# Optimization experiments

Measured on AMD Instinct MI355X. Metric: run time of the kernel, lower is better.

Reference implementation:

```python
import jax, jax.numpy as jnp
import numpy as np

B, S, D = 4, 4096, 1024
H = 16
DH = D // H  # 64, required by the fused kernel


def setup_inputs() -> dict:
    key = jax.random.key(0)
    ks = jax.random.split(key, 5)
    scale = 1.0 / np.sqrt(D)  # xavier-ish init scale for square matrices
    return {
        "x": jax.random.normal(ks[0], (B, S, D), dtype=jnp.float32),
        "Wq": jax.random.normal(ks[1], (D, D), dtype=jnp.float32) * scale,
        "Wk": jax.random.normal(ks[2], (D, D), dtype=jnp.float32) * scale,
        "Wv": jax.random.normal(ks[3], (D, D), dtype=jnp.float32) * scale,
        "Wo": jax.random.normal(ks[4], (D, D), dtype=jnp.float32) * scale,
    }


def reference(x, Wq, Wk, Wv, Wo):
    # Fused QKV projection + linear (non-softmax) attention.
    # Q = x Wq, K = x Wk, V = x Wv, split into H heads of size DH.
    b, s, d = x.shape
    h, dh = H, d // H

    def to_heads(t):
        return t.reshape(b, s, h, dh).transpose(0, 2, 1, 3)  # [B,H,S,dh]

    q = to_heads(jnp.einsum("bsd,de->bse", x, Wq))
    k = to_heads(jnp.einsum("bsd,de->bse", x, Wk))
    v = to_heads(jnp.einsum("bsd,de->bse", x, Wv))

    # Linear attention: O(S * dh^2) per head, never materializes [S,S].
    # out = (1/sqrt(dh)) * Q @ (K^T V)
    scale = 1.0 / jnp.sqrt(jnp.asarray(dh, dtype=x.dtype))
    kv = jnp.einsum("bhsd,bhse->bhde", k, v)          # [B,H,dh,dh]
    out = jnp.einsum("bhsd,bhde->bhse", q, kv) * scale  # [B,H,S,dh]

    # kernel output [B,H,S,dh] -> transpose(1,2) -> view [B,S,D]
    out = out.transpose(0, 2, 1, 3).reshape(b, s, d)
    # out_proj: nn.Linear(D, D, bias=False) -> x @ W.T
    return jnp.einsum("bsd,ed->bse", out, Wo)
```

## Files before the change

### kernel.cpp

```cpp
#include <hip/hip_runtime.h>

typedef unsigned short u16;
typedef unsigned int u32;
typedef u16 u16x8 __attribute__((ext_vector_type(8)));
typedef u16 u16x4 __attribute__((ext_vector_type(4)));
typedef __bf16 bf16x8 __attribute__((ext_vector_type(8)));
typedef float f32x4 __attribute__((ext_vector_type(4)));

__device__ __forceinline__ u16 f2bf(float f) {
    u32 u = __builtin_bit_cast(u32, f);
    u32 r = (u + 0x7fffu + ((u >> 16) & 1u)) >> 16;
    return (u16)r;
}
__device__ __forceinline__ void async16(const u16* g, u16* lds_base) {
    __builtin_amdgcn_global_load_lds(
        (const __attribute__((address_space(1))) void*)g,
        (__attribute__((address_space(3))) void*)lds_base, 16, 0, 0);
}
template <bool SW>
__device__ __forceinline__ f32x4 mf(bf16x8 a, bf16x8 b, f32x4 c) {
    if constexpr (SW) return __builtin_amdgcn_mfma_f32_16x16x32_bf16(b, a, c, 0, 0, 0);
    else              return __builtin_amdgcn_mfma_f32_16x16x32_bf16(a, b, c, 0, 0, 0);
}

__global__ void cvt3_f32_bf16(const float* __restrict__ x, u16* __restrict__ xb,
                              const float* __restrict__ wq, u16* __restrict__ wqb,
                              const float* __restrict__ wo, u16* __restrict__ wob) {
    const int bid = blockIdx.x;
    const float* src; u16* dst; long base;
    if (bid < 8192)      { src = x;  dst = xb;  base = bid; }
    else if (bid < 8704) { src = wq; dst = wqb; base = bid - 8192; }
    else                 { src = wo; dst = wob; base = bid - 8704; }
    const long idx = (base * 256 + threadIdx.x) * 8;
    float4 a = *(const float4*)(src + idx);
    float4 b = *(const float4*)(src + idx + 4);
    u16x8 o;
    o[0] = f2bf(a.x); o[1] = f2bf(a.y); o[2] = f2bf(a.z); o[3] = f2bf(a.w);
    o[4] = f2bf(b.x); o[5] = f2bf(b.y); o[6] = f2bf(b.z); o[7] = f2bf(b.w);
    *(u16x8*)(dst + idx) = o;
}

__global__ void transpose_cvt(const float* __restrict__ W0, const float* __restrict__ W1,
                              u16* __restrict__ WT) {
    __shared__ float tile[32][33];
    const float* W = (blockIdx.z == 0) ? W0 : W1;
    int n0 = blockIdx.x * 32, k0 = blockIdx.y * 32;
    int tx = threadIdx.x, ty = threadIdx.y;
#pragma unroll
    for (int r = 0; r < 4; ++r)
        tile[ty + 8 * r][tx] = W[(size_t)(k0 + ty + 8 * r) * 1024 + n0 + tx];
    __syncthreads();
#pragma unroll
    for (int r = 0; r < 4; ++r) {
        int n = n0 + ty + 8 * r;
        WT[((size_t)blockIdx.z * 1024 + n) * 1024 + k0 + tx] = f2bf(tile[tx][ty + 8 * r]);
    }
}

#define BAR __builtin_amdgcn_s_barrier()
#define WAITLGK do { asm volatile("s_waitcnt lgkmcnt(0)" ::: "memory"); \
                     __builtin_amdgcn_sched_barrier(0); } while (0)
#define PRIO1 __builtin_amdgcn_s_setprio(1)
#define PRIO0 __builtin_amdgcn_s_setprio(0)
#define VM(n) asm volatile("s_waitcnt vmcnt(" #n ")" ::: "memory")

#define As SM[0]
#define Bs SM[1]

#define LDA(buf, mh) do { _Pragma("unroll") for (int mi = 0; mi < 4; ++mi) { \
    const int rA = (wm * 128 + (mh) * 64 + mi * 16 + frow) * 64; \
    aF[mi][0] = *(const bf16x8*)&As[buf][rA + xs0]; \
    aF[mi][1] = *(const bf16x8*)&As[buf][rA + xs1]; } } while (0)

#define LDB(buf, nh) do { _Pragma("unroll") for (int ni = 0; ni < 2; ++ni) { \
    const int rB = (wn * 64 + (nh) * 32 + ni * 16 + frow) * 64; \
    bF[(nh) * 2 + ni][0] = *(const bf16x8*)&Bs[buf][rB + xs0]; \
    bF[(nh) * 2 + ni][1] = *(const bf16x8*)&Bs[buf][rB + xs1]; } } while (0)

#define MFQ(mh, nh) do { _Pragma("unroll") for (int mi = 0; mi < 4; ++mi) \
  _Pragma("unroll") for (int ni = 0; ni < 2; ++ni) \
  _Pragma("unroll") for (int s = 0; s < 2; ++s) \
    acc[(mh) * 4 + mi][(nh) * 2 + ni] = mf<SW>( \
        aF[mi][s], bF[(nh) * 2 + ni][s], acc[(mh) * 4 + mi][(nh) * 2 + ni]); } while (0)

#define TILE4(buf, S2, S3, S4, W1, W2, WV) \
  LDA(buf, 0); LDB(buf, 0); BAR; WAITLGK; PRIO1; MFQ(0, 0); PRIO0; W1; BAR; \
  LDB(buf, 1); S2; BAR; WAITLGK; PRIO1; MFQ(0, 1); PRIO0; W2; BAR; \
  LDA(buf, 1); S3; BAR; WAITLGK; PRIO1; MFQ(1, 1); PRIO0; BAR; \
  S4; BAR; WAITLGK; PRIO1; MFQ(1, 0); PRIO0; WV; BAR;

template <typename OutT, bool KVMODE>
__global__ __launch_bounds__(512, 2) void gemm8p(
    const u16* __restrict__ A, int lda,
    const u16* __restrict__ Bt, int ldb,
    OutT* __restrict__ Cq, int ldc, int K, int nTN,
    size_t btStrideB, u16* __restrict__ Kt, u16* __restrict__ Vt) {
    constexpr bool SW = !KVMODE;
    __shared__ u16 SM[2][2][256 * 64];
    const int tid = threadIdx.x;
    const int wid = tid >> 6, lane = tid & 63;
    const int wm = wid >> 2, wn = wid & 3;

    const int nwg = gridDim.x;
    const int orig = blockIdx.x;
    const int id = (orig & 7) * (nwg >> 3) + (orig >> 3);
    const size_t mBase = (size_t)(id / nTN) * 256;
    const size_t nBase = (size_t)(id % nTN) * 256;

    if (!KVMODE) Bt += (mBase >> 12) * btStrideB;

    const int srow = lane >> 3;
    const int scol = (((lane & 7) ^ (srow & 7)) * 8);

    auto stageH = [&](int buf, int isB, int h, int kt) {
        const u16* g = isB ? Bt : A;
        const int ld = isB ? ldb : lda;
        const size_t rb = isB ? nBase : mBase;
        u16* lds = isB ? Bs[buf] : As[buf];
#pragma unroll
        for (int j = 0; j < 2; ++j) {
            const int rowL = isB ? ((wid >> 1) * 64 + h * 32 + (wid & 1) * 16 + j * 8)
                                 : ((wid >> 2) * 128 + h * 64 + (wid & 3) * 16 + j * 8);
            async16(g + (rb + rowL + srow) * (size_t)ld + (size_t)kt * 64 + scol,
                    lds + rowL * 64);
        }
    };

    const int frow = lane & 15;
    const int xs0 = (((lane >> 4)) ^ (frow & 7)) * 8;
    const int xs1 = ((4 + (lane >> 4)) ^ (frow & 7)) * 8;

    f32x4 acc[8][4] = {};
    bf16x8 aF[4][2], bF[4][2];

#pragma unroll
    for (int h = 0; h < 2; ++h) { stageH(0, 0, h, 0); stageH(0, 1, h, 0); }
#pragma unroll
    for (int h = 0; h < 2; ++h) { stageH(1, 0, h, 1); stageH(1, 1, h, 1); }
    VM(8);
    BAR;

    const int np = K >> 7;
    for (int p = 0; p < np - 1; ++p) {
        const int k2 = 2 * p + 2, k3 = 2 * p + 3;
        TILE4(0,
              { stageH(0, 0, 0, k2); stageH(0, 1, 0, k2); },
              stageH(0, 1, 1, k2),
              stageH(0, 0, 1, k2),
              VM(10), VM(12), VM(12));
        TILE4(1,
              { stageH(1, 0, 0, k3); stageH(1, 1, 0, k3); },
              stageH(1, 1, 1, k3),
              stageH(1, 0, 1, k3),
              VM(10), VM(12), VM(12));
    }
    TILE4(0, , , , , , VM(0));
    TILE4(1, , , , , , );

    const int rb4 = (lane >> 4) * 4;
    const int cx = lane & 15;
    if (!KVMODE) {
#pragma unroll
        for (int m = 0; m < 8; ++m) {
            const size_t row = mBase + wm * 128 + m * 16 + cx;
#pragma unroll
            for (int n = 0; n < 4; ++n) {
                const size_t col = nBase + wn * 64 + n * 16 + rb4;
                *(float4*)&Cq[row * (size_t)ldc + col] =
                    *(float4*)&acc[m][n];
            }
        }
    } else {
        __syncthreads();
        u16* T = &SM[0][0][0];
        const int nLoc = (int)(nBase & 1023);
#pragma unroll
        for (int n = 0; n < 4; ++n) {
            const int colL = wn * 64 + n * 16 + cx;
#pragma unroll
            for (int m = 0; m < 8; ++m) {
                const int R = wm * 128 + m * 16 + rb4;
                u16x4 v;
                v[0] = f2bf(acc[m][n][0]); v[1] = f2bf(acc[m][n][1]);
                v[2] = f2bf(acc[m][n][2]); v[3] = f2bf(acc[m][n][3]);
                const int byteoff = colL * 512 + ((((R >> 3) ^ (colL & 31)) << 4) | ((R & 7) << 1));
                *(u16x4*)((char*)T + byteoff) = v;
            }
        }
        __syncthreads();
        const int b = (int)(mBase >> 12);
        u16* KV = ((nBase >> 10) == 0 ? Kt : Vt);
        const int j = lane & 31;
#pragma unroll
        for (int u = 0; u < 16; ++u) {
            const int iLoc = wid * 32 + u * 2 + (lane >> 5);
            const int byteoff = iLoc * 512 + ((j ^ (iLoc & 31)) << 4);
            const int gcol = nLoc + iLoc;
            u16* dst = KV + (((size_t)(b * 16 + (gcol >> 6)) * 64 + (gcol & 63)) << 12)
                          + (mBase & 4095) + j * 8;
            *(u16x8*)dst = *(const u16x8*)((char*)T + byteoff);
        }
    }
}

__global__ __launch_bounds__(256, 2) void gemm128(
    const u16* __restrict__ A, int lda,
    const u16* __restrict__ Bt, int ldb,
    u16* __restrict__ C, int ldc, int K) {
    __shared__ u16 A2[2][128 * 64];
    __shared__ u16 B2[2][128 * 64];
    const int tid = threadIdx.x, w = tid >> 6, lane = tid & 63;
    const int wr = w >> 1, wc = w & 1;
    const size_t mBase = (size_t)blockIdx.y * 128;
    const size_t nBase = (size_t)blockIdx.x * 128;
    const int lr = lane >> 3;
    const int scol = ((lane & 7) ^ lr) * 8;

    auto stage = [&](int buf, int kt) {
#pragma unroll
        for (int c = 0; c < 2; ++c) {
            const u16* g = c ? Bt : A;
            const int ld = c ? ldb : lda;
            const size_t rb = c ? nBase : mBase;
            u16* lds = c ? B2[buf] : A2[buf];
#pragma unroll
            for (int jj = 0; jj < 4; ++jj) {
                const int rowL = jj * 32 + w * 8;
                async16(g + (rb + rowL + lr) * (size_t)ld + (size_t)kt * 64 + scol,
                        lds + rowL * 64);
            }
        }
    };

    const int frow = lane & 15;
    const int xs0 = ((lane >> 4) ^ (frow & 7)) * 8;
    const int xs1 = ((4 + (lane >> 4)) ^ (frow & 7)) * 8;
    f32x4 acc[4][4] = {};

    stage(0, 0);
    __syncthreads();
    const int nk = K >> 6;
    for (int kt = 0; kt < nk; ++kt) {
        const int cur = kt & 1;
        if (kt + 1 < nk) stage(cur ^ 1, kt + 1);
        bf16x8 bF[4][2];
#pragma unroll
        for (int n = 0; n < 4; ++n) {
            const int rB = (wc * 64 + n * 16 + frow) * 64;
            bF[n][0] = *(const bf16x8*)&B2[cur][rB + xs0];
            bF[n][1] = *(const bf16x8*)&B2[cur][rB + xs1];
        }
#pragma unroll
        for (int m = 0; m < 4; ++m) {
            const int rA = (wr * 64 + m * 16 + frow) * 64;
            bf16x8 a0 = *(const bf16x8*)&A2[cur][rA + xs0];
            bf16x8 a1 = *(const bf16x8*)&A2[cur][rA + xs1];
#pragma unroll
            for (int n = 0; n < 4; ++n) {
                acc[m][n] = mf<true>(a0, bF[n][0], acc[m][n]);
                acc[m][n] = mf<true>(a1, bF[n][1], acc[m][n]);
            }
        }
        __syncthreads();
    }
    const int rb4 = (lane >> 4) * 4, cx = lane & 15;
#pragma unroll
    for (int m = 0; m < 4; ++m) {
        const size_t row = mBase + wr * 64 + m * 16 + cx;
#pragma unroll
        for (int n = 0; n < 4; ++n) {
            const size_t col = nBase + wc * 64 + n * 16 + rb4;
            u16x4 v;
            v[0] = f2bf(acc[m][n][0]); v[1] = f2bf(acc[m][n][1]);
            v[2] = f2bf(acc[m][n][2]); v[3] = f2bf(acc[m][n][3]);
            *(u16x4*)&C[row * (size_t)ldc + col] = v;
        }
    }
}

__global__ __launch_bounds__(256, 2) void kv_gemm(
    const u16* __restrict__ Kt, const u16* __restrict__ Vt, float* __restrict__ P) {
    __shared__ u16 Ks[64 * 64];
    __shared__ u16 Vs[64 * 64];
    const int chunk = blockIdx.x, bh = blockIdx.y;
    const int tid = threadIdx.x, w = tid >> 6, lane = tid & 63;
    const int srow = lane >> 3;
    const int scol = ((lane & 7) ^ srow) * 8;
    const int frow = lane & 15;
    const int xs0 = ((lane >> 4) ^ (frow & 7)) * 8;
    const int xs1 = ((4 + (lane >> 4)) ^ (frow & 7)) * 8;
    const size_t base = (size_t)bh * 64 * 4096 + (size_t)chunk * 512;
    f32x4 acc[4] = {};
    for (int kk = 0; kk < 8; ++kk) {
        __syncthreads();
#pragma unroll
        for (int j = 0; j < 2; ++j) {
            const int row = w * 16 + j * 8;
            async16(Kt + base + (size_t)(row + srow) * 4096 + kk * 64 + scol, &Ks[row * 64]);
            async16(Vt + base + (size_t)(row + srow) * 4096 + kk * 64 + scol, &Vs[row * 64]);
        }
        asm volatile("s_waitcnt vmcnt(0)" ::: "memory");
        __syncthreads();
        bf16x8 a0 = *(const bf16x8*)&Ks[(w * 16 + frow) * 64 + xs0];
        bf16x8 a1 = *(const bf16x8*)&Ks[(w * 16 + frow) * 64 + xs1];
#pragma unroll
        for (int n = 0; n < 4; ++n) {
            bf16x8 b0 = *(const bf16x8*)&Vs[(n * 16 + frow) * 64 + xs0];
            bf16x8 b1 = *(const bf16x8*)&Vs[(n * 16 + frow) * 64 + xs1];
            acc[n] = mf<false>(a0, b0, acc[n]);
            acc[n] = mf<false>(a1, b1, acc[n]);
        }
    }
    const int rb4 = (lane >> 4) * 4, cx = lane & 15;
    float* p = P + ((size_t)chunk * 64 + bh) * 4096;
#pragma unroll
    for (int n = 0; n < 4; ++n)
#pragma unroll
        for (int r = 0; r < 4; ++r)
            p[(w * 16 + rb4 + r) * 64 + n * 16 + cx] = acc[n][r];
}

__global__ void kv_reduce(const float* __restrict__ P, u16* __restrict__ kvb) {
    const int bh = blockIdx.x, t = threadIdx.x;
    for (int idx = t; idx < 4096; idx += 256) {
        float s = 0.f;
#pragma unroll
        for (int c = 0; c < 8; ++c) s += P[((size_t)c * 64 + bh) * 4096 + idx];
        kvb[(size_t)bh * 4096 + idx] = f2bf(s * 0.125f);
    }
}

__global__ __launch_bounds__(256, 2) void w2_gemm(
    const u16* __restrict__ Wob, const u16* __restrict__ kvb, u16* __restrict__ W2t) {
    __shared__ u16 Aw[256 * 64];
    __shared__ u16 Bw[64 * 64];
    const int eT = blockIdx.x, h = blockIdx.y, b = blockIdx.z;
    const int tid = threadIdx.x, w = tid >> 6, lane = tid & 63;
    const int srow = lane >> 3;
    const int scol = ((lane & 7) ^ srow) * 8;
#pragma unroll
    for (int j = 0; j < 8; ++j) {
        const int row = w * 64 + j * 8;
        async16(Wob + (size_t)(eT * 256 + row + srow) * 1024 + h * 64 + scol, &Aw[row * 64]);
    }
#pragma unroll
    for (int j = 0; j < 2; ++j) {
        const int row = w * 16 + j * 8;
        async16(kvb + ((size_t)(b * 16 + h) * 64 + row + srow) * 64 + scol, &Bw[row * 64]);
    }
    asm volatile("s_waitcnt vmcnt(0)" ::: "memory");
    __syncthreads();
    const int frow = lane & 15;
    const int xs0 = ((lane >> 4) ^ (frow & 7)) * 8;
    const int xs1 = ((4 + (lane >> 4)) ^ (frow & 7)) * 8;
    f32x4 acc[4][4] = {};
#pragma unroll
    for (int m = 0; m < 4; ++m) {
        bf16x8 a0 = *(const bf16x8*)&Aw[(w * 64 + m * 16 + frow) * 64 + xs0];
        bf16x8 a1 = *(const bf16x8*)&Aw[(w * 64 + m * 16 + frow) * 64 + xs1];
#pragma unroll
        for (int n = 0; n < 4; ++n) {
            bf16x8 b0 = *(const bf16x8*)&Bw[(n * 16 + frow) * 64 + xs0];
            bf16x8 b1 = *(const bf16x8*)&Bw[(n * 16 + frow) * 64 + xs1];
            acc[m][n] = mf<false>(a0, b0, acc[m][n]);
            acc[m][n] = mf<false>(a1, b1, acc[m][n]);
        }
    }
    const int rb4 = (lane >> 4) * 4, cx = lane & 15;
    u16* out = W2t + (size_t)b * 1048576;
#pragma unroll
    for (int m = 0; m < 4; ++m)
#pragma unroll
        for (int n = 0; n < 4; ++n)
#pragma unroll
            for (int r = 0; r < 4; ++r)
                out[(size_t)(eT * 256 + w * 64 + m * 16 + rb4 + r) * 1024 + h * 64 + n * 16 + cx] =
                    f2bf(acc[m][n][r]);
}

extern "C" void kernel_launch(void* const* d_in, const int* in_sizes, int n_in,
                              void* d_out, int out_size, void* d_ws, size_t ws_size,
                              hipStream_t stream) {
    const float* x  = (const float*)d_in[0];
    const float* Wq = (const float*)d_in[1];
    const float* Wk = (const float*)d_in[2];
    const float* Wv = (const float*)d_in[3];
    const float* Wo = (const float*)d_in[4];
    float* out = (float*)d_out;
    char* ws = (char*)d_ws;

    u16*   xb    = (u16*)(ws);
    u16*   Kt    = (u16*)(ws + 33554432);
    u16*   Vt    = (u16*)(ws + 67108864);
    u16*   WkvT  = (u16*)(ws + 100663296);
    u16*   Wqb   = (u16*)(ws + 104857600);
    u16*   Wob   = (u16*)(ws + 106954752);
    float* Pkv   = (float*)(ws + 109051904);
    u16*   kvb   = (u16*)(ws + 117440512);
    u16*   W2t   = (u16*)(ws + 117964800);
    u16*   W3T   = (u16*)(ws + 126353408);

    cvt3_f32_bf16<<<9216, 256, 0, stream>>>(x, xb, Wq, Wqb, Wo, Wob);
    transpose_cvt<<<dim3(32, 32, 2), dim3(32, 8), 0, stream>>>(Wk, Wv, WkvT);

    gemm8p<u16, true><<<512, 512, 0, stream>>>(xb, 1024, WkvT, 1024, (u16*)nullptr, 0,
                                               1024, 8, 0, Kt, Vt);

    kv_gemm<<<dim3(8, 64), 256, 0, stream>>>(Kt, Vt, Pkv);
    kv_reduce<<<64, 256, 0, stream>>>(Pkv, kvb);
    w2_gemm<<<dim3(4, 16, 4), 256, 0, stream>>>(Wob, kvb, W2t);

    gemm128<<<dim3(8, 32), 256, 0, stream>>>(W2t, 1024, Wqb, 1024, W3T, 1024, 1024);

    gemm8p<float, false><<<256, 512, 0, stream>>>(xb, 1024, W3T, 1024, out, 1024, 1024, 4,
                                                  1048576, nullptr, nullptr);
}
```

Measured before the change: 175.3 us.

## Compute per-head KV via the x^T x Gram matrix instead of materializing K and V

Replaces the large K/V projection GEMM plus the chunked K^T V reduction with a reassociated chain. It builds the per-batch Gram matrix G = x^T x from a transposed bf16 copy of x, then computes Wk^T G and multiplies by per-head slices of Wv to get kv. This halves the FLOPs of the dominant projection stage and removes the large K/V intermediates and the partial-sum buffer. The cost is a new transpose-and-convert pass over x, a K=4096 GEMM run through the simpler 128-tile kernel with only 256 blocks, and an extra bf16 rounding of G that may change accuracy.

```diff
diff --git a/kernel.cpp b/kernel.cpp
--- a/kernel.cpp
+++ b/kernel.cpp
@@ -23,14 +23,41 @@
     else              return __builtin_amdgcn_mfma_f32_16x16x32_bf16(a, b, c, 0, 0, 0);
 }
 
-__global__ void cvt3_f32_bf16(const float* __restrict__ x, u16* __restrict__ xb,
-                              const float* __restrict__ wq, u16* __restrict__ wqb,
+#define BAR __builtin_amdgcn_s_barrier()
+#define WAITLGK do { asm volatile("s_waitcnt lgkmcnt(0)" ::: "memory"); \
+                     __builtin_amdgcn_sched_barrier(0); } while (0)
+#define PRIO1 __builtin_amdgcn_s_setprio(1)
+#define PRIO0 __builtin_amdgcn_s_setprio(0)
+#define VM(n) asm volatile("s_waitcnt vmcnt(" #n ")" ::: "memory")
+
+__global__ void xpose_cvt(const float* __restrict__ x, u16* __restrict__ xb,
+                          u16* __restrict__ xbT) {
+    __shared__ u16 tile[32][33];
+    const int s0 = blockIdx.y * 32, n0 = blockIdx.x * 32;
+    const int tx = threadIdx.x, ty = threadIdx.y;
+#pragma unroll
+    for (int r = 0; r < 4; ++r) {
+        const int s = s0 + ty + 8 * r;
+        const u16 bv = f2bf(x[(size_t)s * 1024 + n0 + tx]);
+        xb[(size_t)s * 1024 + n0 + tx] = bv;
+        tile[ty + 8 * r][tx] = bv;
+    }
+    __syncthreads();
+    const int b = s0 >> 12;
+    const int sl = s0 & 4095;
+#pragma unroll
+    for (int r = 0; r < 4; ++r) {
+        const int n = n0 + ty + 8 * r;
+        xbT[((size_t)b * 1024 + n) * 4096 + sl + tx] = tile[tx][ty + 8 * r];
+    }
+}
+
+__global__ void cvt2_f32_bf16(const float* __restrict__ wq, u16* __restrict__ wqb,
                               const float* __restrict__ wo, u16* __restrict__ wob) {
     const int bid = blockIdx.x;
-    const float* src; u16* dst; long base;
-    if (bid < 8192)      { src = x;  dst = xb;  base = bid; }
-    else if (bid < 8704) { src = wq; dst = wqb; base = bid - 8192; }
-    else                 { src = wo; dst = wob; base = bid - 8704; }
+    const float* src = bid < 512 ? wq : wo;
+    u16* dst = bid < 512 ? wqb : wob;
+    const long base = bid < 512 ? bid : bid - 512;
     const long idx = (base * 256 + threadIdx.x) * 8;
     float4 a = *(const float4*)(src + idx);
     float4 b = *(const float4*)(src + idx + 4);
@@ -57,12 +84,83 @@
     }
 }
 
-#define BAR __builtin_amdgcn_s_barrier()
-#define WAITLGK do { asm volatile("s_waitcnt lgkmcnt(0)" ::: "memory"); \
-                     __builtin_amdgcn_sched_barrier(0); } while (0)
-#define PRIO1 __builtin_amdgcn_s_setprio(1)
-#define PRIO0 __builtin_amdgcn_s_setprio(0)
-#define VM(n) asm volatile("s_waitcnt vmcnt(" #n ")" ::: "memory")
+__global__ __launch_bounds__(256, 2) void gemm128(
+    const u16* __restrict__ A, int lda,
+    const u16* __restrict__ Bt, int ldb,
+    u16* __restrict__ C, int ldc, int K,
+    size_t aMask, size_t btStrideB) {
+    __shared__ u16 A2[2][128 * 64];
+    __shared__ u16 B2[2][128 * 64];
+    const int tid = threadIdx.x, w = tid >> 6, lane = tid & 63;
+    const int wr = w >> 1, wc = w & 1;
+    const size_t mBase = (size_t)blockIdx.y * 128;
+    const size_t nBase = (size_t)blockIdx.x * 128;
+    const size_t mA = mBase & aMask;
+    Bt += (mBase >> 10) * btStrideB;
+    const int lr = lane >> 3;
+    const int scol = ((lane & 7) ^ lr) * 8;
+
+    auto stage = [&](int buf, int kt) {
+#pragma unroll
+        for (int c = 0; c < 2; ++c) {
+            const u16* g = c ? Bt : A;
+            const int ld = c ? ldb : lda;
+            const size_t rb = c ? nBase : mA;
+            u16* lds = c ? B2[buf] : A2[buf];
+#pragma unroll
+            for (int jj = 0; jj < 4; ++jj) {
+                const int rowL = jj * 32 + w * 8;
+                async16(g + (rb + rowL + lr) * (size_t)ld + (size_t)kt * 64 + scol,
+                        lds + rowL * 64);
+            }
+        }
+    };
+
+    const int frow = lane & 15;
+    const int xs0 = ((lane >> 4) ^ (frow & 7)) * 8;
+    const int xs1 = ((4 + (lane >> 4)) ^ (frow & 7)) * 8;
+    f32x4 acc[4][4] = {};
+
+    stage(0, 0);
+    __syncthreads();
+    const int nk = K >> 6;
+    for (int kt = 0; kt < nk; ++kt) {
+        const int cur = kt & 1;
+        if (kt + 1 < nk) stage(cur ^ 1, kt + 1);
+        bf16x8 bF[4][2];
+#pragma unroll
+        for (int n = 0; n < 4; ++n) {
+            const int rB = (wc * 64 + n * 16 + frow) * 64;
+            bF[n][0] = *(const bf16x8*)&B2[cur][rB + xs0];
+            bF[n][1] = *(const bf16x8*)&B2[cur][rB + xs1];
+        }
+#pragma unroll
+        for (int m = 0; m < 4; ++m) {
+            const int rA = (wr * 64 + m * 16 + frow) * 64;
+            bf16x8 a0 = *(const bf16x8*)&A2[cur][rA + xs0];
+            bf16x8 a1 = *(const bf16x8*)&A2[cur][rA + xs1];
+#pragma unroll
+            for (int n = 0; n < 4; ++n) {
+                acc[m][n] = mf<true>(a0, bF[n][0], acc[m][n]);
+                acc[m][n] = mf<true>(a1, bF[n][1], acc[m][n]);
+            }
+        }
+        __syncthreads();
+    }
+    const int rb4 = (lane >> 4) * 4, cx = lane & 15;
+#pragma unroll
+    for (int m = 0; m < 4; ++m) {
+        const size_t row = mBase + wr * 64 + m * 16 + cx;
+#pragma unroll
+        for (int n = 0; n < 4; ++n) {
+            const size_t col = nBase + wc * 64 + n * 16 + rb4;
+            u16x4 v;
+            v[0] = f2bf(acc[m][n][0]); v[1] = f2bf(acc[m][n][1]);
+            v[2] = f2bf(acc[m][n][2]); v[3] = f2bf(acc[m][n][3]);
+            *(u16x4*)&C[row * (size_t)ldc + col] = v;
+        }
+    }
+}
 
 #define As SM[0]
 #define Bs SM[1]
@@ -80,7 +178,7 @@
 #define MFQ(mh, nh) do { _Pragma("unroll") for (int mi = 0; mi < 4; ++mi) \
   _Pragma("unroll") for (int ni = 0; ni < 2; ++ni) \
   _Pragma("unroll") for (int s = 0; s < 2; ++s) \
-    acc[(mh) * 4 + mi][(nh) * 2 + ni] = mf<SW>( \
+    acc[(mh) * 4 + mi][(nh) * 2 + ni] = mf<true>( \
         aF[mi][s], bF[(nh) * 2 + ni][s], acc[(mh) * 4 + mi][(nh) * 2 + ni]); } while (0)
 
 #define TILE4(buf, S2, S3, S4, W1, W2, WV) \
@@ -89,13 +187,11 @@
   LDA(buf, 1); S3; BAR; WAITLGK; PRIO1; MFQ(1, 1); PRIO0; BAR; \
   S4; BAR; WAITLGK; PRIO1; MFQ(1, 0); PRIO0; WV; BAR;
 
-template <typename OutT, bool KVMODE>
 __global__ __launch_bounds__(512, 2) void gemm8p(
     const u16* __restrict__ A, int lda,
     const u16* __restrict__ Bt, int ldb,
-    OutT* __restrict__ Cq, int ldc, int K, int nTN,
-    size_t btStrideB, u16* __restrict__ Kt, u16* __restrict__ Vt) {
-    constexpr bool SW = !KVMODE;
+    float* __restrict__ Cq, int ldc, int K, int nTN,
+    size_t btStrideB) {
     __shared__ u16 SM[2][2][256 * 64];
     const int tid = threadIdx.x;
     const int wid = tid >> 6, lane = tid & 63;
@@ -107,7 +203,7 @@
     const size_t mBase = (size_t)(id / nTN) * 256;
     const size_t nBase = (size_t)(id % nTN) * 256;
 
-    if (!KVMODE) Bt += (mBase >> 12) * btStrideB;
+    Bt += (mBase >> 12) * btStrideB;
 
     const int srow = lane >> 3;
     const int scol = (((lane & 7) ^ (srow & 7)) * 8);
@@ -159,147 +255,40 @@
 
     const int rb4 = (lane >> 4) * 4;
     const int cx = lane & 15;
-    if (!KVMODE) {
-#pragma unroll
-        for (int m = 0; m < 8; ++m) {
-            const size_t row = mBase + wm * 128 + m * 16 + cx;
-#pragma unroll
-            for (int n = 0; n < 4; ++n) {
-                const size_t col = nBase + wn * 64 + n * 16 + rb4;
-                *(float4*)&Cq[row * (size_t)ldc + col] =
-                    *(float4*)&acc[m][n];
-            }
-        }
-    } else {
-        __syncthreads();
-        u16* T = &SM[0][0][0];
-        const int nLoc = (int)(nBase & 1023);
-#pragma unroll
-        for (int n = 0; n < 4; ++n) {
-            const int colL = wn * 64 + n * 16 + cx;
-#pragma unroll
-            for (int m = 0; m < 8; ++m) {
-                const int R = wm * 128 + m * 16 + rb4;
-                u16x4 v;
-                v[0] = f2bf(acc[m][n][0]); v[1] = f2bf(acc[m][n][1]);
-                v[2] = f2bf(acc[m][n][2]); v[3] = f2bf(acc[m][n][3]);
-                const int byteoff = colL * 512 + ((((R >> 3) ^ (colL & 31)) << 4) | ((R & 7) << 1));
-                *(u16x4*)((char*)T + byteoff) = v;
-            }
-        }
-        __syncthreads();
-        const int b = (int)(mBase >> 12);
-        u16* KV = ((nBase >> 10) == 0 ? Kt : Vt);
-        const int j = lane & 31;
-#pragma unroll
-        for (int u = 0; u < 16; ++u) {
-            const int iLoc = wid * 32 + u * 2 + (lane >> 5);
-            const int byteoff = iLoc * 512 + ((j ^ (iLoc & 31)) << 4);
-            const int gcol = nLoc + iLoc;
-            u16* dst = KV + (((size_t)(b * 16 + (gcol >> 6)) * 64 + (gcol & 63)) << 12)
-                          + (mBase & 4095) + j * 8;
-            *(u16x8*)dst = *(const u16x8*)((char*)T + byteoff);
-        }
-    }
-}
-
-__global__ __launch_bounds__(256, 2) void gemm128(
-    const u16* __restrict__ A, int lda,
-    const u16* __restrict__ Bt, int ldb,
-    u16* __restrict__ C, int ldc, int K) {
-    __shared__ u16 A2[2][128 * 64];
-    __shared__ u16 B2[2][128 * 64];
-    const int tid = threadIdx.x, w = tid >> 6, lane = tid & 63;
-    const int wr = w >> 1, wc = w & 1;
-    const size_t mBase = (size_t)blockIdx.y * 128;
-    const size_t nBase = (size_t)blockIdx.x * 128;
-    const int lr = lane >> 3;
-    const int scol = ((lane & 7) ^ lr) * 8;
-
-    auto stage = [&](int buf, int kt) {
-#pragma unroll
-        for (int c = 0; c < 2; ++c) {
-            const u16* g = c ? Bt : A;
-            const int ld = c ? ldb : lda;
-            const size_t rb = c ? nBase : mBase;
-            u16* lds = c ? B2[buf] : A2[buf];
-#pragma unroll
-            for (int jj = 0; jj < 4; ++jj) {
-                const int rowL = jj * 32 + w * 8;
-                async16(g + (rb + rowL + lr) * (size_t)ld + (size_t)kt * 64 + scol,
-                        lds + rowL * 64);
-            }
-        }
-    };
-
-    const int frow = lane & 15;
-    const int xs0 = ((lane >> 4) ^ (frow & 7)) * 8;
-    const int xs1 = ((4 + (lane >> 4)) ^ (frow & 7)) * 8;
-    f32x4 acc[4][4] = {};
-
-    stage(0, 0);
-    __syncthreads();
-    const int nk = K >> 6;
-    for (int kt = 0; kt < nk; ++kt) {
-        const int cur = kt & 1;
-        if (kt + 1 < nk) stage(cur ^ 1, kt + 1);
-        bf16x8 bF[4][2];
-#pragma unroll
-        for (int n = 0; n < 4; ++n) {
-            const int rB = (wc * 64 + n * 16 + frow) * 64;
-            bF[n][0] = *(const bf16x8*)&B2[cur][rB + xs0];
-            bF[n][1] = *(const bf16x8*)&B2[cur][rB + xs1];
-        }
-#pragma unroll
-        for (int m = 0; m < 4; ++m) {
-            const int rA = (wr * 64 + m * 16 + frow) * 64;
-            bf16x8 a0 = *(const bf16x8*)&A2[cur][rA + xs0];
-            bf16x8 a1 = *(const bf16x8*)&A2[cur][rA + xs1];
-#pragma unroll
-            for (int n = 0; n < 4; ++n) {
-                acc[m][n] = mf<true>(a0, bF[n][0], acc[m][n]);
-                acc[m][n] = mf<true>(a1, bF[n][1], acc[m][n]);
-            }
-        }
-        __syncthreads();
-    }
-    const int rb4 = (lane >> 4) * 4, cx = lane & 15;
-#pragma unroll
-    for (int m = 0; m < 4; ++m) {
-        const size_t row = mBase + wr * 64 + m * 16 + cx;
-#pragma unroll
-        for (int n = 0; n < 4; ++n) {
-            const size_t col = nBase + wc * 64 + n * 16 + rb4;
-            u16x4 v;
-            v[0] = f2bf(acc[m][n][0]); v[1] = f2bf(acc[m][n][1]);
-            v[2] = f2bf(acc[m][n][2]); v[3] = f2bf(acc[m][n][3]);
-            *(u16x4*)&C[row * (size_t)ldc + col] = v;
-        }
-    }
-}
-
-__global__ __launch_bounds__(256, 2) void kv_gemm(
-    const u16* __restrict__ Kt, const u16* __restrict__ Vt, float* __restrict__ P) {
+#pragma unroll
+    for (int m = 0; m < 8; ++m) {
+        const size_t row = mBase + wm * 128 + m * 16 + cx;
+#pragma unroll
+        for (int n = 0; n < 4; ++n) {
+            const size_t col = nBase + wn * 64 + n * 16 + rb4;
+            *(float4*)&Cq[row * (size_t)ldc + col] = *(float4*)&acc[m][n];
+        }
+    }
+}
+
+__global__ __launch_bounds__(256, 2) void kv_small(
+    const u16* __restrict__ M1v, const u16* __restrict__ WvT, u16* __restrict__ kvb) {
     __shared__ u16 Ks[64 * 64];
     __shared__ u16 Vs[64 * 64];
-    const int chunk = blockIdx.x, bh = blockIdx.y;
+    const int h = blockIdx.x, b = blockIdx.y;
     const int tid = threadIdx.x, w = tid >> 6, lane = tid & 63;
     const int srow = lane >> 3;
     const int scol = ((lane & 7) ^ srow) * 8;
     const int frow = lane & 15;
     const int xs0 = ((lane >> 4) ^ (frow & 7)) * 8;
     const int xs1 = ((4 + (lane >> 4)) ^ (frow & 7)) * 8;
-    const size_t base = (size_t)bh * 64 * 4096 + (size_t)chunk * 512;
+    const u16* Ap = M1v + (size_t)b * 1048576 + (size_t)h * 64 * 1024;
+    const u16* Bp = WvT + (size_t)h * 64 * 1024;
     f32x4 acc[4] = {};
-    for (int kk = 0; kk < 8; ++kk) {
+    for (int kk = 0; kk < 16; ++kk) {
         __syncthreads();
 #pragma unroll
         for (int j = 0; j < 2; ++j) {
             const int row = w * 16 + j * 8;
-            async16(Kt + base + (size_t)(row + srow) * 4096 + kk * 64 + scol, &Ks[row * 64]);
-            async16(Vt + base + (size_t)(row + srow) * 4096 + kk * 64 + scol, &Vs[row * 64]);
-        }
-        asm volatile("s_waitcnt vmcnt(0)" ::: "memory");
+            async16(Ap + (size_t)(row + srow) * 1024 + kk * 64 + scol, &Ks[row * 64]);
+            async16(Bp + (size_t)(row + srow) * 1024 + kk * 64 + scol, &Vs[row * 64]);
+        }
+        VM(0);
         __syncthreads();
         bf16x8 a0 = *(const bf16x8*)&Ks[(w * 16 + frow) * 64 + xs0];
         bf16x8 a1 = *(const bf16x8*)&Ks[(w * 16 + frow) * 64 + xs1];
@@ -312,22 +301,12 @@
         }
     }
     const int rb4 = (lane >> 4) * 4, cx = lane & 15;
-    float* p = P + ((size_t)chunk * 64 + bh) * 4096;
+    u16* p = kvb + ((size_t)(b * 16 + h)) * 4096;
 #pragma unroll
     for (int n = 0; n < 4; ++n)
 #pragma unroll
         for (int r = 0; r < 4; ++r)
-            p[(w * 16 + rb4 + r) * 64 + n * 16 + cx] = acc[n][r];
-}
-
-__global__ void kv_reduce(const float* __restrict__ P, u16* __restrict__ kvb) {
-    const int bh = blockIdx.x, t = threadIdx.x;
-    for (int idx = t; idx < 4096; idx += 256) {
-        float s = 0.f;
-#pragma unroll
-        for (int c = 0; c < 8; ++c) s += P[((size_t)c * 64 + bh) * 4096 + idx];
-        kvb[(size_t)bh * 4096 + idx] = f2bf(s * 0.125f);
-    }
+            p[(w * 16 + rb4 + r) * 64 + n * 16 + cx] = f2bf(acc[n][r] * 0.125f);
 }
 
 __global__ __launch_bounds__(256, 2) void w2_gemm(
@@ -348,7 +327,7 @@
         const int row = w * 16 + j * 8;
         async16(kvb + ((size_t)(b * 16 + h) * 64 + row + srow) * 64 + scol, &Bw[row * 64]);
     }
-    asm volatile("s_waitcnt vmcnt(0)" ::: "memory");
+    VM(0);
     __syncthreads();
     const int frow = lane & 15;
     const int xs0 = ((lane >> 4) ^ (frow & 7)) * 8;
@@ -389,29 +368,30 @@
     float* out = (float*)d_out;
     char* ws = (char*)d_ws;
 
-    u16*   xb    = (u16*)(ws);
-    u16*   Kt    = (u16*)(ws + 33554432);
-    u16*   Vt    = (u16*)(ws + 67108864);
-    u16*   WkvT  = (u16*)(ws + 100663296);
-    u16*   Wqb   = (u16*)(ws + 104857600);
-    u16*   Wob   = (u16*)(ws + 106954752);
-    float* Pkv   = (float*)(ws + 109051904);
-    u16*   kvb   = (u16*)(ws + 117440512);
-    u16*   W2t   = (u16*)(ws + 117964800);
-    u16*   W3T   = (u16*)(ws + 126353408);
-
-    cvt3_f32_bf16<<<9216, 256, 0, stream>>>(x, xb, Wq, Wqb, Wo, Wob);
+    u16* xb   = (u16*)(ws);
+    u16* xbT  = (u16*)(ws + 33554432);
+    u16* G    = (u16*)(ws + 67108864);
+    u16* M1v  = (u16*)(ws + 75497472);
+    u16* WkvT = (u16*)(ws + 83886080);
+    u16* Wqb  = (u16*)(ws + 88080384);
+    u16* Wob  = (u16*)(ws + 90177536);
+    u16* kvb  = (u16*)(ws + 92274688);
+    u16* W2t  = (u16*)(ws + 92798976);
+    u16* W3T  = (u16*)(ws + 101187584);
+    u16* WkT  = WkvT;
+    u16* WvT  = WkvT + 1048576;
+
+    xpose_cvt<<<dim3(32, 512), dim3(32, 8), 0, stream>>>(x, xb, xbT);
+    cvt2_f32_bf16<<<1024, 256, 0, stream>>>(Wq, Wqb, Wo, Wob);
     transpose_cvt<<<dim3(32, 32, 2), dim3(32, 8), 0, stream>>>(Wk, Wv, WkvT);
 
-    gemm8p<u16, true><<<512, 512, 0, stream>>>(xb, 1024, WkvT, 1024, (u16*)nullptr, 0,
-                                               1024, 8, 0, Kt, Vt);
-
-    kv_gemm<<<dim3(8, 64), 256, 0, stream>>>(Kt, Vt, Pkv);
-    kv_reduce<<<64, 256, 0, stream>>>(Pkv, kvb);
+    gemm128<<<dim3(8, 32), 256, 0, stream>>>(xbT, 4096, xbT, 4096, G, 1024, 4096,
+                                             ~0ULL, 4194304ULL);
+    gemm128<<<dim3(8, 32), 256, 0, stream>>>(WkT, 1024, G, 1024, M1v, 1024, 1024,
+                                             1023ULL, 1048576ULL);
+    kv_small<<<dim3(16, 4), 256, 0, stream>>>(M1v, WvT, kvb);
     w2_gemm<<<dim3(4, 16, 4), 256, 0, stream>>>(Wob, kvb, W2t);
-
-    gemm128<<<dim3(8, 32), 256, 0, stream>>>(W2t, 1024, Wqb, 1024, W3T, 1024, 1024);
-
-    gemm8p<float, false><<<256, 512, 0, stream>>>(xb, 1024, W3T, 1024, out, 1024, 1024, 4,
-                                                  1048576, nullptr, nullptr);
-}
+    gemm128<<<dim3(8, 32), 256, 0, stream>>>(W2t, 1024, Wqb, 1024, W3T, 1024, 1024,
+                                             ~0ULL, 0ULL);
+    gemm8p<<<256, 512, 0, stream>>>(xb, 1024, W3T, 1024, out, 1024, 1024, 4, 1048576ULL);
+}
```

New measurement: 198.2 us. 1.13x slower.
